# Kernel optimization log

Hardware: AMD Instinct MI355X
Metric: run time of the kernel (lower is better)

The kernel has to match this reference:

```python
import jax, jax.numpy as jnp
import numpy as np

LN_EPS = 1e-5

def setup_inputs() -> dict:
    key = jax.random.key(0)
    ks = jax.random.split(key, 8)
    E, F = 500000, 128
    in_right = jax.random.normal(ks[0], (E, F), dtype=jnp.float32)
    in_left = jax.random.normal(ks[1], (E, F), dtype=jnp.float32)
    # MLP params (torch Linear default init scale ~ 1/sqrt(fan_in))
    W1 = jax.random.normal(ks[2], (2 * F, F), dtype=jnp.float32) / np.sqrt(2 * F)
    b1 = jax.random.normal(ks[3], (F,), dtype=jnp.float32) / np.sqrt(2 * F)
    W2 = jax.random.normal(ks[4], (F, F), dtype=jnp.float32) / np.sqrt(F)
    b2 = jax.random.normal(ks[5], (F,), dtype=jnp.float32) / np.sqrt(F)
    gamma = jnp.ones((F,), dtype=jnp.float32)
    beta = jnp.zeros((F,), dtype=jnp.float32)
    return {"in_right": in_right, "in_left": in_left, "W1": W1, "b1": b1,
            "W2": W2, "b2": b2, "gamma": gamma, "beta": beta}

def reference(in_right, in_left, W1, b1, W2, b2, gamma, beta):
    # msg: [2E, 2F] = stack of (left||right) and (right||left)
    in_lr = jnp.concatenate((in_left, in_right), axis=1)
    in_rl = jnp.concatenate((in_right, in_left), axis=1)
    msg = jnp.concatenate((in_lr, in_rl), axis=0)
    h = jax.nn.relu(msg @ W1 + b1)
    h = jax.nn.relu(h @ W2 + b2)
    # LayerNorm over last dim
    mu = jnp.mean(h, axis=-1, keepdims=True)
    var = jnp.var(h, axis=-1, keepdims=True)
    h = (h - mu) * jax.lax.rsqrt(var + LN_EPS) * gamma + beta
    n_edges = in_right.shape[0]
    return h[:n_edges, :], h[n_edges:, :]
```

## Files before the change

kernel.cpp:

```cpp
#include <hip/hip_runtime.h>
#include <hip/hip_bf16.h>

#define LN_EPS 1e-5f

typedef __attribute__((ext_vector_type(8))) short bf16x8;
typedef __attribute__((ext_vector_type(4))) float f32x4;

__device__ __forceinline__ short f2bf(float x) {
    union { float f; unsigned u; } v; v.f = x;
    unsigned r = v.u + 0x7fff + ((v.u >> 16) & 1);
    return (short)(r >> 16);
}

#define IN_STRIDE 528
#define H_STRIDE  272

__global__ __launch_bounds__(256, 2) void mpnn_mfma(
    const float* __restrict__ inR, const float* __restrict__ inL,
    const float* __restrict__ W1, const float* __restrict__ b1,
    const float* __restrict__ W2, const float* __restrict__ b2,
    const float* __restrict__ gamma, const float* __restrict__ beta,
    float* __restrict__ out, int E, int niters)
{
    __shared__ __align__(16) char inA[32 * IN_STRIDE];
    __shared__ __align__(16) char hbuf[64 * H_STRIDE];
    __shared__ float2 lnp[4][4][16];

    const int tid  = threadIdx.x;
    const int lane = tid & 63;
    const int wave = tid >> 6;
    const int r    = lane & 15;
    const int q    = lane >> 4;

    bf16x8 A1[2][8], A2[2][4];
    float4 b1v[2], b2v[2], gv[2], bv[2];
#pragma unroll
    for (int t = 0; t < 2; ++t) {
        const int fr = wave * 32 + t * 16 + r;
#pragma unroll
        for (int c = 0; c < 8; ++c)
#pragma unroll
            for (int i = 0; i < 8; ++i)
                A1[t][c][i] = f2bf(W1[(c * 32 + q * 8 + i) * 128 + fr]);
#pragma unroll
        for (int c = 0; c < 4; ++c)
#pragma unroll
            for (int i = 0; i < 8; ++i)
                A2[t][c][i] = f2bf(W2[(c * 32 + q * 8 + i) * 128 + fr]);
        const int fq = wave * 32 + t * 16 + q * 4;
        b1v[t] = *(const float4*)(b1 + fq);
        b2v[t] = *(const float4*)(b2 + fq);
        gv[t]  = *(const float4*)(gamma + fq);
        bv[t]  = *(const float4*)(beta + fq);
    }

    for (int it = blockIdx.x; it < niters; it += gridDim.x) {
        const int e0 = it * 32;
        __syncthreads();

#pragma unroll
        for (int j = 0; j < 4; ++j) {
            const int idx = j * 256 + tid;
            const int e  = idx >> 5;
            const int hw = (idx >> 4) & 1;
            const int c8 = idx & 15;
            int ee = e0 + e; if (ee >= E) ee = E - 1;
            const float* src = hw ? inR : inL;
            const float4 v0 = *(const float4*)(src + (long)ee * 128 + c8 * 8);
            const float4 v1 = *(const float4*)(src + (long)ee * 128 + c8 * 8 + 4);
            bf16x8 s;
            s[0] = f2bf(v0.x); s[1] = f2bf(v0.y); s[2] = f2bf(v0.z); s[3] = f2bf(v0.w);
            s[4] = f2bf(v1.x); s[5] = f2bf(v1.y); s[6] = f2bf(v1.z); s[7] = f2bf(v1.w);
            *(bf16x8*)(&inA[e * IN_STRIDE + hw * 256 + c8 * 16]) = s;
        }
        __syncthreads();

        f32x4 accL[2][2], accR[2][2];
#pragma unroll
        for (int t = 0; t < 2; ++t)
#pragma unroll
            for (int u = 0; u < 2; ++u) {
                accL[t][u] = f32x4{0.f, 0.f, 0.f, 0.f};
                accR[t][u] = f32x4{0.f, 0.f, 0.f, 0.f};
            }
#pragma unroll
        for (int c = 0; c < 8; ++c) {
            const bf16x8 x0 = *(const bf16x8*)(&inA[r        * IN_STRIDE + c * 64 + q * 16]);
            const bf16x8 x1 = *(const bf16x8*)(&inA[(16 + r) * IN_STRIDE + c * 64 + q * 16]);
            const int crl = (c + 4) & 7;
#pragma unroll
            for (int t = 0; t < 2; ++t) {
                accL[t][0] = __builtin_amdgcn_mfma_f32_16x16x32_bf16(A1[t][c],   x0, accL[t][0], 0, 0, 0);
                accL[t][1] = __builtin_amdgcn_mfma_f32_16x16x32_bf16(A1[t][c],   x1, accL[t][1], 0, 0, 0);
                accR[t][0] = __builtin_amdgcn_mfma_f32_16x16x32_bf16(A1[t][crl], x0, accR[t][0], 0, 0, 0);
                accR[t][1] = __builtin_amdgcn_mfma_f32_16x16x32_bf16(A1[t][crl], x1, accR[t][1], 0, 0, 0);
            }
        }

#pragma unroll
        for (int t = 0; t < 2; ++t) {
            const int fb = wave * 32 + t * 16 + q * 4;
#pragma unroll
            for (int v = 0; v < 4; ++v) {
                const f32x4 a = (v < 2) ? accL[t][v] : accR[t][v - 2];
                short4 s;
                s.x = f2bf(fmaxf(a[0] + b1v[t].x, 0.f));
                s.y = f2bf(fmaxf(a[1] + b1v[t].y, 0.f));
                s.z = f2bf(fmaxf(a[2] + b1v[t].z, 0.f));
                s.w = f2bf(fmaxf(a[3] + b1v[t].w, 0.f));
                *(short4*)(&hbuf[(v * 16 + r) * H_STRIDE + fb * 2]) = s;
            }
        }
        __syncthreads();

        f32x4 acc2[2][4];
#pragma unroll
        for (int t = 0; t < 2; ++t)
#pragma unroll
            for (int v = 0; v < 4; ++v) acc2[t][v] = f32x4{0.f, 0.f, 0.f, 0.f};
#pragma unroll
        for (int c = 0; c < 4; ++c) {
#pragma unroll
            for (int v = 0; v < 4; ++v) {
                const bf16x8 y = *(const bf16x8*)(&hbuf[(v * 16 + r) * H_STRIDE + c * 64 + q * 16]);
#pragma unroll
                for (int t = 0; t < 2; ++t)
                    acc2[t][v] = __builtin_amdgcn_mfma_f32_16x16x32_bf16(A2[t][c], y, acc2[t][v], 0, 0, 0);
            }
        }

        float s1[4] = {0.f, 0.f, 0.f, 0.f}, s2[4] = {0.f, 0.f, 0.f, 0.f};
#pragma unroll
        for (int t = 0; t < 2; ++t)
#pragma unroll
            for (int v = 0; v < 4; ++v) {
                f32x4 a = acc2[t][v];
                a[0] = fmaxf(a[0] + b2v[t].x, 0.f);
                a[1] = fmaxf(a[1] + b2v[t].y, 0.f);
                a[2] = fmaxf(a[2] + b2v[t].z, 0.f);
                a[3] = fmaxf(a[3] + b2v[t].w, 0.f);
                acc2[t][v] = a;
                s1[v] += a[0] + a[1] + a[2] + a[3];
                s2[v] += a[0] * a[0] + a[1] * a[1] + a[2] * a[2] + a[3] * a[3];
            }
#pragma unroll
        for (int v = 0; v < 4; ++v) {
            s1[v] += __shfl_xor(s1[v], 16);
            s1[v] += __shfl_xor(s1[v], 32);
            s2[v] += __shfl_xor(s2[v], 16);
            s2[v] += __shfl_xor(s2[v], 32);
        }
        if (lane < 16) {
#pragma unroll
            for (int v = 0; v < 4; ++v)
                lnp[wave][v][lane] = make_float2(s1[v], s2[v]);
        }
        __syncthreads();

#pragma unroll
        for (int v = 0; v < 4; ++v) {
            float S1 = 0.f, S2 = 0.f;
#pragma unroll
            for (int w = 0; w < 4; ++w) {
                const float2 p = lnp[w][v][r];
                S1 += p.x; S2 += p.y;
            }
            const float mu  = S1 * (1.f / 128.f);
            const float var = S2 * (1.f / 128.f) - mu * mu;
            const float rs  = rsqrtf(var + LN_EPS);
            const int el = (v & 1) * 16 + r;
            const bool ok = (e0 + el) < E;
            const long orow = ((v < 2) ? 0L : (long)E) + e0 + el;
#pragma unroll
            for (int t = 0; t < 2; ++t) {
                const int fb = wave * 32 + t * 16 + q * 4;
                const f32x4 a = acc2[t][v];
                float4 o;
                o.x = (a[0] - mu) * rs * gv[t].x + bv[t].x;
                o.y = (a[1] - mu) * rs * gv[t].y + bv[t].y;
                o.z = (a[2] - mu) * rs * gv[t].z + bv[t].z;
                o.w = (a[3] - mu) * rs * gv[t].w + bv[t].w;
                if (ok)
                    *(float4*)(out + orow * 128 + fb) = o;
            }
        }
    }
}

extern "C" void kernel_launch(void* const* d_in, const int* in_sizes, int n_in,
                              void* d_out, int out_size, void* d_ws, size_t ws_size,
                              hipStream_t stream) {
    const float* inR   = (const float*)d_in[0];
    const float* inL   = (const float*)d_in[1];
    const float* W1    = (const float*)d_in[2];
    const float* b1    = (const float*)d_in[3];
    const float* W2    = (const float*)d_in[4];
    const float* b2    = (const float*)d_in[5];
    const float* gamma = (const float*)d_in[6];
    const float* beta  = (const float*)d_in[7];
    const int E = in_sizes[0] / 128;

    const int niters = (E + 31) / 32;
    const int grid = niters < 2048 ? niters : 2048;
    mpnn_mfma<<<grid, 256, 0, stream>>>(inR, inL, W1, b1, W2, b2, gamma, beta,
                                        (float*)d_out, E, niters);
}
```

Baseline: 223.8 us.

## Double-buffer input tiles with register prefetch of next iteration

The next tile's global loads and bf16 conversion now go into registers at the start of each iteration. They are written to a second LDS buffer after the epilogue, so memory latency overlaps with the MFMA and LayerNorm work. The grid size is also balanced so every block runs the same number of iterations. The prefetch adds 32 VGPRs for the staging registers and doubles the input LDS, which may hurt occupancy under launch_bounds(256,2).

Result: slower. 267.5 us (+19.5%).

```diff
diff --git a/kernel.cpp b/kernel.cpp
--- a/kernel.cpp
+++ b/kernel.cpp
@@ -22,7 +22,7 @@
     const float* __restrict__ gamma, const float* __restrict__ beta,
     float* __restrict__ out, int E, int niters)
 {
-    __shared__ __align__(16) char inA[32 * IN_STRIDE];
+    __shared__ __align__(16) char inA[2][32 * IN_STRIDE];
     __shared__ __align__(16) char hbuf[64 * H_STRIDE];
     __shared__ float2 lnp[4][4][16];
 
@@ -54,26 +54,44 @@
         bv[t]  = *(const float4*)(beta + fq);
     }
 
-    for (int it = blockIdx.x; it < niters; it += gridDim.x) {
-        const int e0 = it * 32;
-        __syncthreads();
-
+    bf16x8 sreg[4];
+    auto loadcvt = [&](int itx) {
 #pragma unroll
         for (int j = 0; j < 4; ++j) {
             const int idx = j * 256 + tid;
             const int e  = idx >> 5;
             const int hw = (idx >> 4) & 1;
             const int c8 = idx & 15;
-            int ee = e0 + e; if (ee >= E) ee = E - 1;
+            long ee = (long)itx * 32 + e; if (ee >= E) ee = E - 1;
             const float* src = hw ? inR : inL;
-            const float4 v0 = *(const float4*)(src + (long)ee * 128 + c8 * 8);
-            const float4 v1 = *(const float4*)(src + (long)ee * 128 + c8 * 8 + 4);
+            const float4 v0 = *(const float4*)(src + ee * 128 + c8 * 8);
+            const float4 v1 = *(const float4*)(src + ee * 128 + c8 * 8 + 4);
             bf16x8 s;
             s[0] = f2bf(v0.x); s[1] = f2bf(v0.y); s[2] = f2bf(v0.z); s[3] = f2bf(v0.w);
             s[4] = f2bf(v1.x); s[5] = f2bf(v1.y); s[6] = f2bf(v1.z); s[7] = f2bf(v1.w);
-            *(bf16x8*)(&inA[e * IN_STRIDE + hw * 256 + c8 * 16]) = s;
-        }
-        __syncthreads();
+            sreg[j] = s;
+        }
+    };
+    auto stwrite = [&](int buf) {
+#pragma unroll
+        for (int j = 0; j < 4; ++j) {
+            const int idx = j * 256 + tid;
+            const int e  = idx >> 5;
+            const int hw = (idx >> 4) & 1;
+            const int c8 = idx & 15;
+            *(bf16x8*)(&inA[buf][e * IN_STRIDE + hw * 256 + c8 * 16]) = sreg[j];
+        }
+    };
+
+    int it  = blockIdx.x;
+    int cur = 0;
+    if (it < niters) { loadcvt(it); stwrite(0); }
+    __syncthreads();
+
+    for (; it < niters; it += gridDim.x) {
+        const int e0  = it * 32;
+        const int itn = it + gridDim.x;
+        if (itn < niters) loadcvt(itn);
 
         f32x4 accL[2][2], accR[2][2];
 #pragma unroll
@@ -85,8 +103,8 @@
             }
 #pragma unroll
         for (int c = 0; c < 8; ++c) {
-            const bf16x8 x0 = *(const bf16x8*)(&inA[r        * IN_STRIDE + c * 64 + q * 16]);
-            const bf16x8 x1 = *(const bf16x8*)(&inA[(16 + r) * IN_STRIDE + c * 64 + q * 16]);
+            const bf16x8 x0 = *(const bf16x8*)(&inA[cur][r        * IN_STRIDE + c * 64 + q * 16]);
+            const bf16x8 x1 = *(const bf16x8*)(&inA[cur][(16 + r) * IN_STRIDE + c * 64 + q * 16]);
             const int crl = (c + 4) & 7;
 #pragma unroll
             for (int t = 0; t < 2; ++t) {
@@ -184,6 +202,10 @@
                     *(float4*)(out + orow * 128 + fb) = o;
             }
         }
+
+        if (itn < niters) stwrite(cur ^ 1);
+        __syncthreads();
+        cur ^= 1;
     }
 }
 
@@ -201,7 +223,8 @@
     const int E = in_sizes[0] / 128;
 
     const int niters = (E + 31) / 32;
-    const int grid = niters < 2048 ? niters : 2048;
+    const int d = (niters + 2047) / 2048;
+    const int grid = (niters + d - 1) / d;
     mpnn_mfma<<<grid, 256, 0, stream>>>(inR, inL, W1, b1, W2, b2, gamma, beta,
                                         (float*)d_out, E, niters);
 }
```

## Double per-iteration edge tile to 64 and balance grid over iterations

Applied to the files above, without the earlier changes.

Each block iteration now processes 64 edges instead of 32, so every register-resident weight fragment is reused across twice as many MFMA operations and each barrier covers more work. Accumulators are merged into a single acc[2][8] array that both GEMM stages reuse. The launch bound's min-blocks hint is dropped, and the grid size is chosen so iterations divide evenly across blocks. The trade-off is more registers and twice the shared memory, which may reduce occupancy and the overlap of global loads.

Measured after the change: 312.1 us. 1.39x slower.

```diff
diff --git a/kernel.cpp b/kernel.cpp
--- a/kernel.cpp
+++ b/kernel.cpp
@@ -15,16 +15,16 @@
 #define IN_STRIDE 528
 #define H_STRIDE  272
 
-__global__ __launch_bounds__(256, 2) void mpnn_mfma(
+__global__ __launch_bounds__(256) void mpnn_mfma(
     const float* __restrict__ inR, const float* __restrict__ inL,
     const float* __restrict__ W1, const float* __restrict__ b1,
     const float* __restrict__ W2, const float* __restrict__ b2,
     const float* __restrict__ gamma, const float* __restrict__ beta,
     float* __restrict__ out, int E, int niters)
 {
-    __shared__ __align__(16) char inA[32 * IN_STRIDE];
-    __shared__ __align__(16) char hbuf[64 * H_STRIDE];
-    __shared__ float2 lnp[4][4][16];
+    __shared__ __align__(16) char inA[64 * IN_STRIDE];
+    __shared__ __align__(16) char hbuf[128 * H_STRIDE];
+    __shared__ float2 lnp[4][8][16];
 
     const int tid  = threadIdx.x;
     const int lane = tid & 63;
@@ -55,11 +55,11 @@
     }
 
     for (int it = blockIdx.x; it < niters; it += gridDim.x) {
-        const int e0 = it * 32;
-        __syncthreads();
-
-#pragma unroll
-        for (int j = 0; j < 4; ++j) {
+        const int e0 = it * 64;
+        __syncthreads();
+
+#pragma unroll
+        for (int j = 0; j < 8; ++j) {
             const int idx = j * 256 + tid;
             const int e  = idx >> 5;
             const int hw = (idx >> 4) & 1;
@@ -75,76 +75,77 @@
         }
         __syncthreads();
 
-        f32x4 accL[2][2], accR[2][2];
+        f32x4 acc[2][8];
 #pragma unroll
         for (int t = 0; t < 2; ++t)
 #pragma unroll
-            for (int u = 0; u < 2; ++u) {
-                accL[t][u] = f32x4{0.f, 0.f, 0.f, 0.f};
-                accR[t][u] = f32x4{0.f, 0.f, 0.f, 0.f};
-            }
+            for (int v = 0; v < 8; ++v)
+                acc[t][v] = f32x4{0.f, 0.f, 0.f, 0.f};
 #pragma unroll
         for (int c = 0; c < 8; ++c) {
-            const bf16x8 x0 = *(const bf16x8*)(&inA[r        * IN_STRIDE + c * 64 + q * 16]);
-            const bf16x8 x1 = *(const bf16x8*)(&inA[(16 + r) * IN_STRIDE + c * 64 + q * 16]);
+            bf16x8 x[4];
+#pragma unroll
+            for (int u = 0; u < 4; ++u)
+                x[u] = *(const bf16x8*)(&inA[(u * 16 + r) * IN_STRIDE + c * 64 + q * 16]);
             const int crl = (c + 4) & 7;
 #pragma unroll
-            for (int t = 0; t < 2; ++t) {
-                accL[t][0] = __builtin_amdgcn_mfma_f32_16x16x32_bf16(A1[t][c],   x0, accL[t][0], 0, 0, 0);
-                accL[t][1] = __builtin_amdgcn_mfma_f32_16x16x32_bf16(A1[t][c],   x1, accL[t][1], 0, 0, 0);
-                accR[t][0] = __builtin_amdgcn_mfma_f32_16x16x32_bf16(A1[t][crl], x0, accR[t][0], 0, 0, 0);
-                accR[t][1] = __builtin_amdgcn_mfma_f32_16x16x32_bf16(A1[t][crl], x1, accR[t][1], 0, 0, 0);
-            }
+            for (int t = 0; t < 2; ++t)
+#pragma unroll
+                for (int u = 0; u < 4; ++u) {
+                    acc[t][u]     = __builtin_amdgcn_mfma_f32_16x16x32_bf16(A1[t][c],   x[u], acc[t][u],     0, 0, 0);
+                    acc[t][u + 4] = __builtin_amdgcn_mfma_f32_16x16x32_bf16(A1[t][crl], x[u], acc[t][u + 4], 0, 0, 0);
+                }
         }
 
 #pragma unroll
         for (int t = 0; t < 2; ++t) {
-            const int fb = wave * 32 + t * 16 + q * 4;
-#pragma unroll
-            for (int v = 0; v < 4; ++v) {
-                const f32x4 a = (v < 2) ? accL[t][v] : accR[t][v - 2];
+            const int fq = wave * 32 + t * 16 + q * 4;
+#pragma unroll
+            for (int v = 0; v < 8; ++v) {
+                const f32x4 a = acc[t][v];
                 short4 s;
                 s.x = f2bf(fmaxf(a[0] + b1v[t].x, 0.f));
                 s.y = f2bf(fmaxf(a[1] + b1v[t].y, 0.f));
                 s.z = f2bf(fmaxf(a[2] + b1v[t].z, 0.f));
                 s.w = f2bf(fmaxf(a[3] + b1v[t].w, 0.f));
-                *(short4*)(&hbuf[(v * 16 + r) * H_STRIDE + fb * 2]) = s;
-            }
-        }
-        __syncthreads();
-
-        f32x4 acc2[2][4];
+                *(short4*)(&hbuf[(v * 16 + r) * H_STRIDE + fq * 2]) = s;
+            }
+        }
+        __syncthreads();
+
 #pragma unroll
         for (int t = 0; t < 2; ++t)
 #pragma unroll
-            for (int v = 0; v < 4; ++v) acc2[t][v] = f32x4{0.f, 0.f, 0.f, 0.f};
+            for (int v = 0; v < 8; ++v) acc[t][v] = f32x4{0.f, 0.f, 0.f, 0.f};
 #pragma unroll
         for (int c = 0; c < 4; ++c) {
 #pragma unroll
-            for (int v = 0; v < 4; ++v) {
+            for (int v = 0; v < 8; ++v) {
                 const bf16x8 y = *(const bf16x8*)(&hbuf[(v * 16 + r) * H_STRIDE + c * 64 + q * 16]);
 #pragma unroll
                 for (int t = 0; t < 2; ++t)
-                    acc2[t][v] = __builtin_amdgcn_mfma_f32_16x16x32_bf16(A2[t][c], y, acc2[t][v], 0, 0, 0);
-            }
-        }
-
-        float s1[4] = {0.f, 0.f, 0.f, 0.f}, s2[4] = {0.f, 0.f, 0.f, 0.f};
+                    acc[t][v] = __builtin_amdgcn_mfma_f32_16x16x32_bf16(A2[t][c], y, acc[t][v], 0, 0, 0);
+            }
+        }
+
+        float s1[8], s2[8];
+#pragma unroll
+        for (int v = 0; v < 8; ++v) { s1[v] = 0.f; s2[v] = 0.f; }
 #pragma unroll
         for (int t = 0; t < 2; ++t)
 #pragma unroll
-            for (int v = 0; v < 4; ++v) {
-                f32x4 a = acc2[t][v];
+            for (int v = 0; v < 8; ++v) {
+                f32x4 a = acc[t][v];
                 a[0] = fmaxf(a[0] + b2v[t].x, 0.f);
                 a[1] = fmaxf(a[1] + b2v[t].y, 0.f);
                 a[2] = fmaxf(a[2] + b2v[t].z, 0.f);
                 a[3] = fmaxf(a[3] + b2v[t].w, 0.f);
-                acc2[t][v] = a;
+                acc[t][v] = a;
                 s1[v] += a[0] + a[1] + a[2] + a[3];
                 s2[v] += a[0] * a[0] + a[1] * a[1] + a[2] * a[2] + a[3] * a[3];
             }
 #pragma unroll
-        for (int v = 0; v < 4; ++v) {
+        for (int v = 0; v < 8; ++v) {
             s1[v] += __shfl_xor(s1[v], 16);
             s1[v] += __shfl_xor(s1[v], 32);
             s2[v] += __shfl_xor(s2[v], 16);
@@ -152,13 +153,13 @@
         }
         if (lane < 16) {
 #pragma unroll
-            for (int v = 0; v < 4; ++v)
+            for (int v = 0; v < 8; ++v)
                 lnp[wave][v][lane] = make_float2(s1[v], s2[v]);
         }
         __syncthreads();
 
 #pragma unroll
-        for (int v = 0; v < 4; ++v) {
+        for (int v = 0; v < 8; ++v) {
             float S1 = 0.f, S2 = 0.f;
 #pragma unroll
             for (int w = 0; w < 4; ++w) {
@@ -168,20 +169,20 @@
             const float mu  = S1 * (1.f / 128.f);
             const float var = S2 * (1.f / 128.f) - mu * mu;
             const float rs  = rsqrtf(var + LN_EPS);
-            const int el = (v & 1) * 16 + r;
+            const int el = (v & 3) * 16 + r;
             const bool ok = (e0 + el) < E;
-            const long orow = ((v < 2) ? 0L : (long)E) + e0 + el;
+            const long orow = ((v < 4) ? 0L : (long)E) + e0 + el;
 #pragma unroll
             for (int t = 0; t < 2; ++t) {
-                const int fb = wave * 32 + t * 16 + q * 4;
-                const f32x4 a = acc2[t][v];
+                const int fq = wave * 32 + t * 16 + q * 4;
+                const f32x4 a = acc[t][v];
                 float4 o;
                 o.x = (a[0] - mu) * rs * gv[t].x + bv[t].x;
                 o.y = (a[1] - mu) * rs * gv[t].y + bv[t].y;
                 o.z = (a[2] - mu) * rs * gv[t].z + bv[t].z;
                 o.w = (a[3] - mu) * rs * gv[t].w + bv[t].w;
                 if (ok)
-                    *(float4*)(out + orow * 128 + fb) = o;
+                    *(float4*)(out + orow * 128 + fq) = o;
             }
         }
     }
@@ -200,8 +201,9 @@
     const float* beta  = (const float*)d_in[7];
     const int E = in_sizes[0] / 128;
 
-    const int niters = (E + 31) / 32;
-    const int grid = niters < 2048 ? niters : 2048;
+    const int niters = (E + 63) / 64;
+    const int d = (niters + 2047) / 2048;
+    const int grid = (niters + d - 1) / d;
     mpnn_mfma<<<grid, 256, 0, stream>>>(inR, inL, W1, b1, W2, b2, gamma, beta,
                                         (float*)d_out, E, niters);
 }
```
